# Kernel optimization log

Measured on AMD Instinct MI355X. Metric: run time of the kernel, lower is better.

## Reference

```python
import math
import jax, jax.numpy as jnp
import numpy as np

WIN = 8
NUM_HEADS = 8

def _rel_pos_index(win):
    coords = np.stack(np.meshgrid(np.arange(win), np.arange(win), indexing='ij'))
    cf = coords.reshape(2, -1)
    rel = cf[:, :, None] - cf[:, None, :]
    rel = rel.transpose(1, 2, 0).copy()
    rel[:, :, 0] += win - 1
    rel[:, :, 1] += win - 1
    rel[:, :, 0] *= 2 * win - 1
    return rel.sum(-1)  # [N, N]

def _shift_mask(H, W, win, Ho, Wo):
    m = np.zeros((H, W))
    h_slices = (slice(0, -win), slice(-win, -Ho), slice(-Ho, None)) if Ho > 0 else (slice(0, None),)
    w_slices = (slice(0, -win), slice(-win, -Wo), slice(-Wo, None)) if Wo > 0 else (slice(0, None),)
    cnt = 0
    for hs in h_slices:
        for ws in w_slices:
            m[hs, ws] = cnt
            cnt += 1
    mw = m.reshape(H // win, win, W // win, win).transpose(0, 2, 1, 3).reshape(-1, win * win)
    d = mw[:, None, :] - mw[:, :, None]
    return np.where(d != 0, -100.0, 0.0).astype(np.float32)  # [nW, N, N]

def _ln(x, g, b, eps=1e-5):
    mu = jnp.mean(x, axis=-1, keepdims=True)
    var = jnp.mean((x - mu) ** 2, axis=-1, keepdims=True)
    return (x - mu) / jnp.sqrt(var + eps) * g + b

def _win_part(x, win):
    B, H, W, C = x.shape
    x = x.reshape(B, H // win, win, W // win, win, C).transpose(0, 1, 3, 2, 4, 5)
    return x.reshape(-1, win * win, C)

def _win_rev(w, win, H, W):
    C = w.shape[-1]
    B = w.shape[0] // ((H // win) * (W // win))
    x = w.reshape(B, H // win, W // win, win, win, C).transpose(0, 1, 3, 2, 4, 5)
    return x.reshape(B, H, W, C)

def setup_inputs() -> dict:
    key = jax.random.key(0)
    ks = jax.random.split(key, 10)
    B, L, C, hid = 4, 32768, 256, 1024
    s = 0.02
    return {
        'x': jax.random.normal(ks[0], (B, L, C), jnp.float32),
        'norm1_g': jnp.ones((C,), jnp.float32),
        'norm1_b': jnp.zeros((C,), jnp.float32),
        'wq': jax.random.normal(ks[1], (C, C), jnp.float32) * s,
        'bq': jnp.zeros((C,), jnp.float32),
        'wv': jax.random.normal(ks[2], (C, C), jnp.float32) * s,
        'bv': jnp.zeros((C,), jnp.float32),
        'rpb': jax.random.normal(ks[3], (225, NUM_HEADS), jnp.float32) * s,
        'wproj': jax.random.normal(ks[4], (C, C), jnp.float32) * s,
        'bproj': jnp.zeros((C,), jnp.float32),
        'norm2_g': jnp.ones((C,), jnp.float32),
        'norm2_b': jnp.zeros((C,), jnp.float32),
        'w1': jax.random.normal(ks[5], (C, hid), jnp.float32) * s,
        'b1': jnp.zeros((hid,), jnp.float32),
        'dw_k': jax.random.normal(ks[6], (hid, 1, 3, 3), jnp.float32) * s,
        'dw_b': jnp.zeros((hid,), jnp.float32),
        'w2': jax.random.normal(ks[7], (hid, C), jnp.float32) * s,
        'b2': jnp.zeros((C,), jnp.float32),
        'H_offset': 3,
        'W_offset': 5,
    }

def reference(x, norm1_g, norm1_b, wq, bq, wv, bv, rpb, wproj, bproj,
              norm2_g, norm2_b, w1, b1, dw_k, dw_b, w2, b2, H_offset, W_offset):
    B, L, C = x.shape
    H = int(round(math.sqrt(L * 2)))
    W = int(round(math.sqrt(L // 2)))
    win, h = WIN, NUM_HEADS
    hd = C // h
    N = win * win
    nW = (H // win) * (W // win)
    scale = hd ** -0.5

    shortcut = x
    xn = _ln(x, norm1_g, norm1_b)
    q = xn @ wq + bq
    v = xn @ wv + bv
    q = q.reshape(B, H, W, C)
    v = v.reshape(B, H, W, C)
    k = q  # module uses k = q (shared)

    q = jnp.roll(q, (-H_offset, -W_offset), axis=(1, 2))
    k = jnp.roll(k, (-H_offset, -W_offset), axis=(1, 2))
    v = jnp.roll(v, (-H_offset, -W_offset), axis=(1, 2))

    qw = _win_part(q, win).reshape(-1, N, h, hd).transpose(0, 2, 1, 3)
    kw = _win_part(k, win).reshape(-1, N, h, hd).transpose(0, 2, 1, 3)
    vw = _win_part(v, win).reshape(-1, N, h, hd).transpose(0, 2, 1, 3)

    attn = jnp.einsum('bhnd,bhmd->bhnm', qw * scale, kw)
    bias = rpb[jnp.asarray(_rel_pos_index(win).reshape(-1))].reshape(N, N, h).transpose(2, 0, 1)
    attn = attn + bias[None]
    mask = jnp.asarray(_shift_mask(H, W, win, int(H_offset), int(W_offset)))
    attn = (attn.reshape(B, nW, h, N, N) + mask[None, :, None]).reshape(-1, h, N, N)
    attn = jax.nn.softmax(attn, axis=-1)

    y = jnp.einsum('bhnm,bhmd->bhnd', attn, vw).transpose(0, 2, 1, 3).reshape(-1, N, C)
    y = y @ wproj + bproj
    y = _win_rev(y.reshape(-1, win, win, C), win, H, W)
    y = jnp.roll(y, (H_offset, W_offset), axis=(1, 2)).reshape(B, L, C)

    x = shortcut + y

    # LeFF
    xn2 = _ln(x, norm2_g, norm2_b)
    t = jax.nn.gelu(xn2 @ w1 + b1, approximate=False)  # [B, L, hid]
    t = t.reshape(B, H, W, -1).transpose(0, 3, 1, 2)   # NCHW
    t = jax.lax.conv_general_dilated(t, dw_k, (1, 1), 'SAME',
                                     feature_group_count=t.shape[1],
                                     dimension_numbers=('NCHW', 'OIHW', 'NCHW'))
    t = jax.nn.gelu(t + dw_b[None, :, None, None], approximate=False)
    t = t.transpose(0, 2, 3, 1).reshape(B, L, -1)
    t = t @ w2 + b2
    return x + t
```

## Files before the change

kernel.cpp:

```cpp
#include <hip/hip_runtime.h>
#include <stdint.h>
#include <math.h>

#define H_IMG 256
#define W_IMG 128
#define LTOK  32768
#define BATCH 4
#define CDIM  256
#define HIDDIM 1024
#define NHEAD 8
#define HD    32
#define MROWS 131072

typedef __attribute__((ext_vector_type(8))) short short8;
typedef __attribute__((ext_vector_type(4))) float f32x4;

__device__ __forceinline__ float bf2f(unsigned u) {
  union { unsigned u; float f; } c; c.u = u << 16; return c.f;
}
__device__ __forceinline__ unsigned short f2bf(float f) {
  union { float f; unsigned u; } c; c.f = f;
  unsigned r = c.u + 0x7fffu + ((c.u >> 16) & 1u);
  return (unsigned short)(r >> 16);
}
__device__ __forceinline__ float gelu_f(float x) {
  return 0.5f * x * (1.0f + erff(x * 0.70710678118654752f));
}
__device__ __forceinline__ void gload_lds16(const void* g, void* l) {
  __builtin_amdgcn_global_load_lds(
      (const __attribute__((address_space(1))) unsigned int*)g,
      (__attribute__((address_space(3))) unsigned int*)l, 16, 0, 0);
}

__global__ __launch_bounds__(256) void wconv_kernel(
    const float* __restrict__ w, unsigned short* __restrict__ wt, int K, int N) {
  __shared__ float t[32][33];
  const int k0 = blockIdx.x * 32, n0 = blockIdx.y * 32;
  const int tx = threadIdx.x & 31, ty = threadIdx.x >> 5;
#pragma unroll
  for (int i = 0; i < 4; ++i)
    t[ty + 8 * i][tx] = w[(size_t)(k0 + ty + 8 * i) * N + n0 + tx];
  __syncthreads();
#pragma unroll
  for (int i = 0; i < 4; ++i)
    wt[(size_t)(n0 + ty + 8 * i) * K + k0 + tx] = f2bf(t[tx][ty + 8 * i]);
}

__global__ __launch_bounds__(256) void ln_kernel(
    const float* __restrict__ x, const float* __restrict__ g,
    const float* __restrict__ b, unsigned short* __restrict__ out) {
  const int wave = threadIdx.x >> 6;
  const int lane = threadIdx.x & 63;
  const size_t row = (size_t)blockIdx.x * 4 + wave;
  float4 f = ((const float4*)(x + row * CDIM))[lane];
  float s  = f.x + f.y + f.z + f.w;
  float sq = f.x*f.x + f.y*f.y + f.z*f.z + f.w*f.w;
#pragma unroll
  for (int o = 32; o > 0; o >>= 1) { s += __shfl_down(s, o); sq += __shfl_down(sq, o); }
  s = __shfl(s, 0); sq = __shfl(sq, 0);
  const float mu = s * (1.0f / CDIM);
  const float var = sq * (1.0f / CDIM) - mu * mu;
  const float rstd = rsqrtf(var + 1e-5f);
  float4 gg = ((const float4*)g)[lane];
  float4 bb = ((const float4*)b)[lane];
  unsigned short o4[4];
  o4[0] = f2bf((f.x - mu) * rstd * gg.x + bb.x);
  o4[1] = f2bf((f.y - mu) * rstd * gg.y + bb.y);
  o4[2] = f2bf((f.z - mu) * rstd * gg.z + bb.z);
  o4[3] = f2bf((f.w - mu) * rstd * gg.w + bb.w);
  *(uint2*)(out + row * CDIM + lane * 4) = *(uint2*)o4;
}

template<int EPI>
__global__ __launch_bounds__(256) void mgemm(
    const unsigned short* __restrict__ A, const unsigned short* __restrict__ Bt,
    const float* __restrict__ bias, float bscale, const float* __restrict__ res,
    void* __restrict__ outp, int K, int ldc) {
  __shared__ unsigned short As[128][32];
  __shared__ unsigned short Bs[128][32];
  const int tid = threadIdx.x;
  const int w = tid >> 6, lane = tid & 63;
  const int m0 = blockIdx.x * 128, n0 = blockIdx.y * 128;
  const int wm = (w & 1) * 64, wn = (w >> 1) * 64;
  const int srow = lane >> 2;
  const int csrc = (lane & 3) ^ (srow & 3);
  f32x4 acc[4][4];
#pragma unroll
  for (int mi = 0; mi < 4; ++mi)
#pragma unroll
    for (int ni = 0; ni < 4; ++ni)
#pragma unroll
      for (int r = 0; r < 4; ++r) acc[mi][ni][r] = 0.0f;

  const int kg = lane >> 4, ml = lane & 15;
  for (int kk = 0; kk < K; kk += 32) {
#pragma unroll
    for (int i = 0; i < 2; ++i) {
      const int rl = w * 32 + i * 16 + srow;
      gload_lds16(A + (size_t)(m0 + rl) * K + kk + csrc * 8, &As[w * 32 + i * 16][0]);
      gload_lds16(Bt + (size_t)(n0 + rl) * K + kk + csrc * 8, &Bs[w * 32 + i * 16][0]);
    }
    __syncthreads();
    short8 af[4], bg[4];
#pragma unroll
    for (int mi = 0; mi < 4; ++mi) {
      const int r = wm + mi * 16 + ml;
      af[mi] = *(const short8*)&As[r][(kg ^ (r & 3)) * 8];
    }
#pragma unroll
    for (int ni = 0; ni < 4; ++ni) {
      const int r = wn + ni * 16 + ml;
      bg[ni] = *(const short8*)&Bs[r][(kg ^ (r & 3)) * 8];
    }
#pragma unroll
    for (int mi = 0; mi < 4; ++mi)
#pragma unroll
      for (int ni = 0; ni < 4; ++ni)
        acc[mi][ni] = __builtin_amdgcn_mfma_f32_16x16x32_bf16(af[mi], bg[ni], acc[mi][ni], 0, 0, 0);
    __syncthreads();
  }
#pragma unroll
  for (int ni = 0; ni < 4; ++ni) {
    const int n = n0 + wn + ni * 16 + ml;
    const float bn = bias[n] * bscale;
#pragma unroll
    for (int mi = 0; mi < 4; ++mi) {
#pragma unroll
      for (int r = 0; r < 4; ++r) {
        const int m = m0 + wm + mi * 16 + kg * 4 + r;
        const size_t idx = (size_t)m * ldc + n;
        float val = acc[mi][ni][r] + bn;
        if (EPI == 1) {
          ((float*)outp)[idx] = val + res[idx];
        } else if (EPI == 2) {
          ((unsigned short*)outp)[idx] = f2bf(gelu_f(val));
        } else {
          ((unsigned short*)outp)[idx] = f2bf(val);
        }
      }
    }
  }
}

__global__ __launch_bounds__(256, 3) void attn_kernel(
    const unsigned short* __restrict__ q, const unsigned short* __restrict__ v,
    const float* __restrict__ rpb, const int* __restrict__ pHo,
    const int* __restrict__ pWo, unsigned short* __restrict__ yout) {
  __shared__ char wbuf[4][8704];
  __shared__ float bias_w[4][228];
  __shared__ int reg_s[64];
  const int tid = threadIdx.x;
  const int w = tid >> 6, lane = tid & 63;
  const int g = lane >> 4, c = lane & 15;
  const int wb = blockIdx.x;
  const int b = wb >> 9, wloc = wb & 511;
  const int wh = wloc >> 4, ww = wloc & 15;
  const int Ho = pHo[0], Wo = pWo[0];
  const int dy = lane >> 3, dx = lane & 7;
  const int hr = wh * 8 + dy, wr = ww * 8 + dx;
  int ho = hr + Ho; if (ho >= H_IMG) ho -= H_IMG;
  int wo = wr + Wo; if (wo >= W_IMG) wo -= W_IMG;
  const size_t tok = (size_t)b * LTOK + (size_t)ho * W_IMG + wo;
  const bool edge = (wh == (H_IMG / 8 - 1)) || (ww == (W_IMG / 8 - 1));
  if (w == 0) {
    const int rh = (hr < H_IMG - 8) ? 0 : ((hr < H_IMG - Ho) ? 1 : 2);
    const int rw = (wr < W_IMG - 8) ? 0 : ((wr < W_IMG - Wo) ? 1 : 2);
    reg_s[lane] = rh * 3 + rw;
  }
  __syncthreads();

  unsigned short* qh = (unsigned short*)&wbuf[w][0];
  unsigned short* vt = (unsigned short*)&wbuf[w][4096];
  unsigned short* Pp = (unsigned short*)&wbuf[w][0];

  const float scale = 0.17677669529663687f;
  const int dxk = c & 7, dyk0 = c >> 3;
  const int base_l = 112 - dyk0 * 15 - dxk;

  for (int p2 = 0; p2 < 2; ++p2) {
    const int hh = w + 4 * p2;
    const uint4* vp = (const uint4*)(v + tok * CDIM + hh * HD);
    uint4 a0 = vp[0], a1 = vp[1], a2 = vp[2], a3 = vp[3];
#pragma unroll
    for (int i = 0; i < 4; ++i) {
      const int idx = lane + 64 * i;
      if (idx < 225) bias_w[w][idx] = rpb[idx * 8 + hh];
    }
#pragma unroll
    for (int u = 0; u < 4; ++u) {
      const int t2 = u * 16 + (lane >> 2);
      int ho2 = wh * 8 + (t2 >> 3) + Ho; if (ho2 >= H_IMG) ho2 -= H_IMG;
      int wo2 = ww * 8 + (t2 & 7) + Wo;  if (wo2 >= W_IMG) wo2 -= W_IMG;
      const size_t tk = (size_t)b * LTOK + (size_t)ho2 * W_IMG + wo2;
      gload_lds16(q + tk * CDIM + hh * HD + (lane & 3) * 8, &qh[u * 512]);
    }
    {
      unsigned tmp[16] = {a0.x,a0.y,a0.z,a0.w,a1.x,a1.y,a1.z,a1.w,
                          a2.x,a2.y,a2.z,a2.w,a3.x,a3.y,a3.z,a3.w};
#pragma unroll
      for (int d2 = 0; d2 < 16; ++d2) {
        vt[(2 * d2) * 72 + lane]     = (unsigned short)(tmp[d2] & 0xffffu);
        vt[(2 * d2 + 1) * 72 + lane] = (unsigned short)(tmp[d2] >> 16);
      }
    }
    asm volatile("s_waitcnt vmcnt(0)" ::: "memory");
    short8 q4[4];
#pragma unroll
    for (int mi = 0; mi < 4; ++mi)
      q4[mi] = *(const short8*)&qh[(16 * mi + c) * 32 + g * 8];
    short8 vf[2][2];
#pragma unroll
    for (int s2 = 0; s2 < 2; ++s2)
#pragma unroll
      for (int n2 = 0; n2 < 2; ++n2)
        vf[s2][n2] = *(const short8*)&vt[(16 * n2 + c) * 72 + 32 * s2 + 8 * g];
    f32x4 acc[4][4];
#pragma unroll
    for (int mi = 0; mi < 4; ++mi)
#pragma unroll
      for (int nj = 0; nj < 4; ++nj)
#pragma unroll
        for (int r = 0; r < 4; ++r) acc[mi][nj][r] = 0.0f;
#pragma unroll
    for (int mi = 0; mi < 4; ++mi)
#pragma unroll
      for (int nj = 0; nj < 4; ++nj)
        acc[mi][nj] = __builtin_amdgcn_mfma_f32_16x16x32_bf16(q4[mi], q4[nj], acc[mi][nj], 0, 0, 0);
    int regk[4];
    if (edge) {
#pragma unroll
      for (int nj = 0; nj < 4; ++nj) regk[nj] = reg_s[16 * nj + c];
    }
#pragma unroll
    for (int mi = 0; mi < 4; ++mi) {
#pragma unroll
      for (int r = 0; r < 4; ++r) {
        const int qq = 16 * mi + 4 * g + r;
        const int rb = (qq >> 3) * 15 + (qq & 7) + base_l;
        float sv[4];
#pragma unroll
        for (int nj = 0; nj < 4; ++nj)
          sv[nj] = acc[mi][nj][r] * scale + bias_w[w][rb - 30 * nj];
        if (edge) {
          const int regq = reg_s[qq];
#pragma unroll
          for (int nj = 0; nj < 4; ++nj)
            if (regq != regk[nj]) sv[nj] -= 100.0f;
        }
        float mx2 = fmaxf(fmaxf(sv[0], sv[1]), fmaxf(sv[2], sv[3]));
        mx2 = fmaxf(mx2, __shfl_xor(mx2, 1));
        mx2 = fmaxf(mx2, __shfl_xor(mx2, 2));
        mx2 = fmaxf(mx2, __shfl_xor(mx2, 4));
        mx2 = fmaxf(mx2, __shfl_xor(mx2, 8));
        float e0 = __expf(sv[0] - mx2), e1 = __expf(sv[1] - mx2);
        float e2 = __expf(sv[2] - mx2), e3 = __expf(sv[3] - mx2);
        float sm = e0 + e1 + e2 + e3;
        sm += __shfl_xor(sm, 1);
        sm += __shfl_xor(sm, 2);
        sm += __shfl_xor(sm, 4);
        sm += __shfl_xor(sm, 8);
        const float iv = __builtin_amdgcn_rcpf(sm);
        const int rowoff = qq * 64, sw = qq & 7;
        Pp[rowoff + ((dyk0 ^ sw) * 8)       + dxk] = f2bf(e0 * iv);
        Pp[rowoff + (((2 + dyk0) ^ sw) * 8) + dxk] = f2bf(e1 * iv);
        Pp[rowoff + (((4 + dyk0) ^ sw) * 8) + dxk] = f2bf(e2 * iv);
        Pp[rowoff + (((6 + dyk0) ^ sw) * 8) + dxk] = f2bf(e3 * iv);
      }
    }
    f32x4 oacc[4][2];
#pragma unroll
    for (int mi = 0; mi < 4; ++mi)
#pragma unroll
      for (int n2 = 0; n2 < 2; ++n2)
#pragma unroll
        for (int r = 0; r < 4; ++r) oacc[mi][n2][r] = 0.0f;
#pragma unroll
    for (int s2 = 0; s2 < 2; ++s2) {
      short8 pa[4];
#pragma unroll
      for (int mi = 0; mi < 4; ++mi) {
        const int qq2 = 16 * mi + c;
        pa[mi] = *(const short8*)&Pp[qq2 * 64 + (((4 * s2 + g) ^ (qq2 & 7)) * 8)];
      }
#pragma unroll
      for (int mi = 0; mi < 4; ++mi)
#pragma unroll
        for (int n2 = 0; n2 < 2; ++n2)
          oacc[mi][n2] = __builtin_amdgcn_mfma_f32_16x16x32_bf16(pa[mi], vf[s2][n2], oacc[mi][n2], 0, 0, 0);
    }
    unsigned short* Ost = Pp;
#pragma unroll
    for (int mi = 0; mi < 4; ++mi)
#pragma unroll
      for (int n2 = 0; n2 < 2; ++n2)
#pragma unroll
        for (int r = 0; r < 4; ++r)
          Ost[(16 * mi + 4 * g + r) * 40 + 16 * n2 + c] = f2bf(oacc[mi][n2][r]);
    uint4* op = (uint4*)(yout + tok * CDIM + hh * HD);
#pragma unroll
    for (int u = 0; u < 4; ++u)
      op[u] = *(const uint4*)&Ost[lane * 40 + u * 8];
  }
}

__global__ __launch_bounds__(256) void dwconv_kernel(
    const unsigned short* __restrict__ t1b, const float* __restrict__ k9,
    const float* __restrict__ bias, unsigned short* __restrict__ t2b,
    int hr0, int band_rows) {
  const int c = blockIdx.y * 128 + (threadIdx.x & 31) * 4;
  const int tok = blockIdx.x * 8 + (threadIdx.x >> 5);
  const int h = hr0 + (tok >> 7), wcol = tok & 127;
  float wreg[4][9];
#pragma unroll
  for (int j = 0; j < 4; ++j)
#pragma unroll
    for (int tp = 0; tp < 9; ++tp) wreg[j][tp] = k9[(c + j) * 9 + tp];
  const float4 bv = *(const float4*)(bias + c);
  float a0 = 0, a1 = 0, a2 = 0, a3 = 0;
#pragma unroll
  for (int ky = 0; ky < 3; ++ky) {
    const int hy = h + ky - 1;
    if ((unsigned)hy >= (unsigned)H_IMG) continue;
    const int brow = (tok >> 7) + ky;
#pragma unroll
    for (int kx = 0; kx < 3; ++kx) {
      const int wx = wcol + kx - 1;
      if ((unsigned)wx >= (unsigned)W_IMG) continue;
      const ushort4 tv = *(const ushort4*)(
          t1b + ((size_t)(brow * 128 + wx)) * HIDDIM + c);
      const int tp = ky * 3 + kx;
      a0 += bf2f(tv.x) * wreg[0][tp];
      a1 += bf2f(tv.y) * wreg[1][tp];
      a2 += bf2f(tv.z) * wreg[2][tp];
      a3 += bf2f(tv.w) * wreg[3][tp];
    }
  }
  a0 = gelu_f(a0 + bv.x); a1 = gelu_f(a1 + bv.y);
  a2 = gelu_f(a2 + bv.z); a3 = gelu_f(a3 + bv.w);
  unsigned short o[4] = { f2bf(a0), f2bf(a1), f2bf(a2), f2bf(a3) };
  *(uint2*)(t2b + (size_t)tok * HIDDIM + c) = *(uint2*)o;
}

extern "C" void kernel_launch(void* const* d_in, const int* in_sizes, int n_in,
                              void* d_out, int out_size, void* d_ws, size_t ws_size,
                              hipStream_t stream) {
  (void)in_sizes; (void)n_in; (void)out_size; (void)ws_size;
  const float* x     = (const float*)d_in[0];
  const float* n1g   = (const float*)d_in[1];
  const float* n1b   = (const float*)d_in[2];
  const float* wq    = (const float*)d_in[3];
  const float* bq    = (const float*)d_in[4];
  const float* wv    = (const float*)d_in[5];
  const float* bv    = (const float*)d_in[6];
  const float* rpb   = (const float*)d_in[7];
  const float* wproj = (const float*)d_in[8];
  const float* bproj = (const float*)d_in[9];
  const float* n2g   = (const float*)d_in[10];
  const float* n2b   = (const float*)d_in[11];
  const float* w1    = (const float*)d_in[12];
  const float* b1    = (const float*)d_in[13];
  const float* dwk   = (const float*)d_in[14];
  const float* dwb   = (const float*)d_in[15];
  const float* w2    = (const float*)d_in[16];
  const float* b2    = (const float*)d_in[17];
  const int*   pHo   = (const int*)d_in[18];
  const int*   pWo   = (const int*)d_in[19];
  float* out = (float*)d_out;

  char* wsb = (char*)d_ws;
  unsigned short* r0     = (unsigned short*)wsb;
  unsigned short* wqt    = (unsigned short*)(wsb + 67108864ull);
  unsigned short* wvt    = (unsigned short*)(wsb + 67108864ull + 131072ull);
  unsigned short* wprojt = (unsigned short*)(wsb + 67108864ull + 262144ull);
  unsigned short* w1t    = (unsigned short*)(wsb + 67108864ull + 393216ull);
  unsigned short* w2t    = (unsigned short*)(wsb + 67108864ull + 917504ull);
  unsigned short* t1b    = (unsigned short*)(wsb + 68550656ull);
  unsigned short* t2b    = (unsigned short*)(wsb + 68550656ull + 25690112ull);
  unsigned short* vb     = (unsigned short*)d_out;
  unsigned short* qb     = (unsigned short*)((char*)d_out + 67108864ull);

  wconv_kernel<<<dim3(8, 8),  256, 0, stream>>>(wq,    wqt,    CDIM, CDIM);
  wconv_kernel<<<dim3(8, 8),  256, 0, stream>>>(wv,    wvt,    CDIM, CDIM);
  wconv_kernel<<<dim3(8, 8),  256, 0, stream>>>(wproj, wprojt, CDIM, CDIM);
  wconv_kernel<<<dim3(8, 32), 256, 0, stream>>>(w1,    w1t,    CDIM, HIDDIM);
  wconv_kernel<<<dim3(32, 8), 256, 0, stream>>>(w2,    w2t,    HIDDIM, CDIM);

  ln_kernel<<<32768, 256, 0, stream>>>(x, n1g, n1b, r0);
  mgemm<0><<<dim3(1024, 2), 256, 0, stream>>>(r0, wqt, bq, 1.0f, nullptr, qb, CDIM, CDIM);
  mgemm<0><<<dim3(1024, 2), 256, 0, stream>>>(r0, wvt, bv, 1.0f, nullptr, vb, CDIM, CDIM);
  attn_kernel<<<dim3(2048), 256, 0, stream>>>(qb, vb, rpb, pHo, pWo, r0);
  mgemm<1><<<dim3(1024, 2), 256, 0, stream>>>(r0, wprojt, bproj, 1.0f, x, out, CDIM, CDIM);
  ln_kernel<<<32768, 256, 0, stream>>>(out, n2g, n2b, r0);
  for (int bi = 0; bi < BATCH; ++bi) {
    for (int hr0 = 0; hr0 < H_IMG; ) {
      const int br = (H_IMG - hr0 >= 96) ? 96 : (H_IMG - hr0);
      const int r_start = (hr0 > 0) ? hr0 - 1 : 0;
      const int r_end = (hr0 + br <= H_IMG - 1) ? hr0 + br : H_IMG - 1;
      const int nrows = r_end - r_start + 1;
      const unsigned short* Aff1 = r0 + ((size_t)bi * LTOK + (size_t)r_start * W_IMG) * CDIM;
      unsigned short* t1dst = t1b + (size_t)(r_start - hr0 + 1) * W_IMG * HIDDIM;
      mgemm<2><<<dim3(nrows, 8), 256, 0, stream>>>(
          Aff1, w1t, b1, 1.0f, nullptr, t1dst, CDIM, HIDDIM);
      dwconv_kernel<<<dim3(br * 16, 8), 256, 0, stream>>>(t1b, dwk, dwb, t2b, hr0, br);
      const size_t btok = (size_t)bi * LTOK + (size_t)hr0 * W_IMG;
      mgemm<1><<<dim3(br, 2), 256, 0, stream>>>(
          t2b, w2t, b2, 1.0f, out + btok * CDIM, out + btok * CDIM, HIDDIM, CDIM);
      hr0 += br;
    }
  }
}
```

Baseline: 1.635 ms.

## Double-buffer GEMM K loop, write Q/V in window-major layout, drop softmax max

The GEMM main loop now uses two LDS stages so the next K tile is prefetched while MFMAs run on the current one. The Q and V projection GEMMs write their output already shifted and window-partitioned per head (V transposed), and the projection GEMM reads window-ordered rows and scatters them back with the reverse roll. This lets the attention kernel read Q/V fragments straight from global memory without LDS staging or transposes. The softmax also drops the row-max subtraction and applies the normalisation after P@V, which assumes scores stay small enough not to overflow exp.

```diff
diff --git a/kernel.cpp b/kernel.cpp
--- a/kernel.cpp
+++ b/kernel.cpp
@@ -71,13 +71,14 @@
   *(uint2*)(out + row * CDIM + lane * 4) = *(uint2*)o4;
 }
 
-template<int EPI>
+template<int EPI, int PERM>
 __global__ __launch_bounds__(256) void mgemm(
     const unsigned short* __restrict__ A, const unsigned short* __restrict__ Bt,
     const float* __restrict__ bias, float bscale, const float* __restrict__ res,
-    void* __restrict__ outp, int K, int ldc) {
-  __shared__ unsigned short As[128][32];
-  __shared__ unsigned short Bs[128][32];
+    void* __restrict__ outp, int K, int ldc,
+    const int* __restrict__ pHo, const int* __restrict__ pWo) {
+  __shared__ unsigned short As[2][128][32];
+  __shared__ unsigned short Bs[2][128][32];
   const int tid = threadIdx.x;
   const int w = tid >> 6, lane = tid & 63;
   const int m0 = blockIdx.x * 128, n0 = blockIdx.y * 128;
@@ -93,42 +94,88 @@
       for (int r = 0; r < 4; ++r) acc[mi][ni][r] = 0.0f;
 
   const int kg = lane >> 4, ml = lane & 15;
-  for (int kk = 0; kk < K; kk += 32) {
+  const int nt = K >> 5;
+
+  auto STAGE = [&](int kk, int buf) {
 #pragma unroll
     for (int i = 0; i < 2; ++i) {
       const int rl = w * 32 + i * 16 + srow;
-      gload_lds16(A + (size_t)(m0 + rl) * K + kk + csrc * 8, &As[w * 32 + i * 16][0]);
-      gload_lds16(Bt + (size_t)(n0 + rl) * K + kk + csrc * 8, &Bs[w * 32 + i * 16][0]);
-    }
-    __syncthreads();
+      gload_lds16(A + (size_t)(m0 + rl) * K + kk + csrc * 8, &As[buf][w * 32 + i * 16][0]);
+      gload_lds16(Bt + (size_t)(n0 + rl) * K + kk + csrc * 8, &Bs[buf][w * 32 + i * 16][0]);
+    }
+  };
+
+  STAGE(0, 0);
+  for (int t = 0; t < nt; ++t) {
+    const int cur = t & 1;
+    if (t + 1 < nt) {
+      STAGE((t + 1) << 5, cur ^ 1);
+      asm volatile("s_waitcnt vmcnt(4)" ::: "memory");
+    } else {
+      asm volatile("s_waitcnt vmcnt(0)" ::: "memory");
+    }
+    __builtin_amdgcn_s_barrier();
+    __builtin_amdgcn_sched_barrier(0);
     short8 af[4], bg[4];
 #pragma unroll
     for (int mi = 0; mi < 4; ++mi) {
       const int r = wm + mi * 16 + ml;
-      af[mi] = *(const short8*)&As[r][(kg ^ (r & 3)) * 8];
+      af[mi] = *(const short8*)&As[cur][r][(kg ^ (r & 3)) * 8];
     }
 #pragma unroll
     for (int ni = 0; ni < 4; ++ni) {
       const int r = wn + ni * 16 + ml;
-      bg[ni] = *(const short8*)&Bs[r][(kg ^ (r & 3)) * 8];
+      bg[ni] = *(const short8*)&Bs[cur][r][(kg ^ (r & 3)) * 8];
     }
 #pragma unroll
     for (int mi = 0; mi < 4; ++mi)
 #pragma unroll
       for (int ni = 0; ni < 4; ++ni)
         acc[mi][ni] = __builtin_amdgcn_mfma_f32_16x16x32_bf16(af[mi], bg[ni], acc[mi][ni], 0, 0, 0);
-    __syncthreads();
+    __builtin_amdgcn_sched_barrier(0);
+    __builtin_amdgcn_s_barrier();
+  }
+
+  const int Ho = (PERM == 1 || PERM == 2 || PERM == 3) ? pHo[0] : 0;
+  const int Wo = (PERM == 1 || PERM == 2 || PERM == 3) ? pWo[0] : 0;
+  size_t ridx[4][4];
+#pragma unroll
+  for (int mi = 0; mi < 4; ++mi) {
+#pragma unroll
+    for (int r = 0; r < 4; ++r) {
+      const int m = m0 + wm + mi * 16 + kg * 4 + r;
+      if constexpr (PERM == 1 || PERM == 2) {
+        const int bimg = m >> 15, l = m & 32767;
+        const int hq = l >> 7, wq_ = l & 127;
+        int hr = hq - Ho; if (hr < 0) hr += H_IMG;
+        int wr = wq_ - Wo; if (wr < 0) wr += W_IMG;
+        const int win = (hr >> 3) * 16 + (wr >> 3);
+        const int t64 = (hr & 7) * 8 + (wr & 7);
+        ridx[mi][r] = (size_t)(bimg * 512 + win) * 16384 +
+                      (PERM == 1 ? t64 * 32 : t64);
+      } else if constexpr (PERM == 3) {
+        const int bimg = m >> 15, win = (m >> 6) & 511, t64 = m & 63;
+        int h = (win >> 4) * 8 + (t64 >> 3) + Ho; if (h >= H_IMG) h -= H_IMG;
+        int ww_ = (win & 15) * 8 + (t64 & 7) + Wo; if (ww_ >= W_IMG) ww_ -= W_IMG;
+        ridx[mi][r] = ((size_t)(bimg << 15) + h * W_IMG + ww_) * ldc;
+      } else {
+        ridx[mi][r] = (size_t)m * ldc;
+      }
+    }
   }
 #pragma unroll
   for (int ni = 0; ni < 4; ++ni) {
     const int n = n0 + wn + ni * 16 + ml;
     const float bn = bias[n] * bscale;
+    size_t noff;
+    if constexpr (PERM == 1)      noff = (size_t)(n >> 5) * 2048 + (n & 31);
+    else if constexpr (PERM == 2) noff = (size_t)(n >> 5) * 2048 + (n & 31) * 64;
+    else                          noff = (size_t)n;
 #pragma unroll
     for (int mi = 0; mi < 4; ++mi) {
 #pragma unroll
       for (int r = 0; r < 4; ++r) {
-        const int m = m0 + wm + mi * 16 + kg * 4 + r;
-        const size_t idx = (size_t)m * ldc + n;
+        const size_t idx = ridx[mi][r] + noff;
         float val = acc[mi][ni][r] + bn;
         if (EPI == 1) {
           ((float*)outp)[idx] = val + res[idx];
@@ -146,7 +193,7 @@
     const unsigned short* __restrict__ q, const unsigned short* __restrict__ v,
     const float* __restrict__ rpb, const int* __restrict__ pHo,
     const int* __restrict__ pWo, unsigned short* __restrict__ yout) {
-  __shared__ char wbuf[4][8704];
+  __shared__ unsigned short Pb[4][4096];
   __shared__ float bias_w[4][228];
   __shared__ int reg_s[64];
   const int tid = threadIdx.x;
@@ -156,64 +203,40 @@
   const int b = wb >> 9, wloc = wb & 511;
   const int wh = wloc >> 4, ww = wloc & 15;
   const int Ho = pHo[0], Wo = pWo[0];
-  const int dy = lane >> 3, dx = lane & 7;
-  const int hr = wh * 8 + dy, wr = ww * 8 + dx;
-  int ho = hr + Ho; if (ho >= H_IMG) ho -= H_IMG;
-  int wo = wr + Wo; if (wo >= W_IMG) wo -= W_IMG;
-  const size_t tok = (size_t)b * LTOK + (size_t)ho * W_IMG + wo;
   const bool edge = (wh == (H_IMG / 8 - 1)) || (ww == (W_IMG / 8 - 1));
   if (w == 0) {
+    const int dy = lane >> 3, dx = lane & 7;
+    const int hr = wh * 8 + dy, wr = ww * 8 + dx;
     const int rh = (hr < H_IMG - 8) ? 0 : ((hr < H_IMG - Ho) ? 1 : 2);
     const int rw = (wr < W_IMG - 8) ? 0 : ((wr < W_IMG - Wo) ? 1 : 2);
     reg_s[lane] = rh * 3 + rw;
   }
   __syncthreads();
 
-  unsigned short* qh = (unsigned short*)&wbuf[w][0];
-  unsigned short* vt = (unsigned short*)&wbuf[w][4096];
-  unsigned short* Pp = (unsigned short*)&wbuf[w][0];
-
   const float scale = 0.17677669529663687f;
   const int dxk = c & 7, dyk0 = c >> 3;
   const int base_l = 112 - dyk0 * 15 - dxk;
+  const size_t hbase0 = (size_t)(b * 512 + wloc) * 8;
 
   for (int p2 = 0; p2 < 2; ++p2) {
     const int hh = w + 4 * p2;
-    const uint4* vp = (const uint4*)(v + tok * CDIM + hh * HD);
-    uint4 a0 = vp[0], a1 = vp[1], a2 = vp[2], a3 = vp[3];
+    const unsigned short* qh = q + (hbase0 + hh) * 2048;
+    const unsigned short* vh = v + (hbase0 + hh) * 2048;
 #pragma unroll
     for (int i = 0; i < 4; ++i) {
       const int idx = lane + 64 * i;
       if (idx < 225) bias_w[w][idx] = rpb[idx * 8 + hh];
     }
-#pragma unroll
-    for (int u = 0; u < 4; ++u) {
-      const int t2 = u * 16 + (lane >> 2);
-      int ho2 = wh * 8 + (t2 >> 3) + Ho; if (ho2 >= H_IMG) ho2 -= H_IMG;
-      int wo2 = ww * 8 + (t2 & 7) + Wo;  if (wo2 >= W_IMG) wo2 -= W_IMG;
-      const size_t tk = (size_t)b * LTOK + (size_t)ho2 * W_IMG + wo2;
-      gload_lds16(q + tk * CDIM + hh * HD + (lane & 3) * 8, &qh[u * 512]);
-    }
-    {
-      unsigned tmp[16] = {a0.x,a0.y,a0.z,a0.w,a1.x,a1.y,a1.z,a1.w,
-                          a2.x,a2.y,a2.z,a2.w,a3.x,a3.y,a3.z,a3.w};
-#pragma unroll
-      for (int d2 = 0; d2 < 16; ++d2) {
-        vt[(2 * d2) * 72 + lane]     = (unsigned short)(tmp[d2] & 0xffffu);
-        vt[(2 * d2 + 1) * 72 + lane] = (unsigned short)(tmp[d2] >> 16);
-      }
-    }
-    asm volatile("s_waitcnt vmcnt(0)" ::: "memory");
     short8 q4[4];
 #pragma unroll
     for (int mi = 0; mi < 4; ++mi)
-      q4[mi] = *(const short8*)&qh[(16 * mi + c) * 32 + g * 8];
+      q4[mi] = *(const short8*)(qh + (16 * mi + c) * 32 + g * 8);
     short8 vf[2][2];
 #pragma unroll
     for (int s2 = 0; s2 < 2; ++s2)
 #pragma unroll
       for (int n2 = 0; n2 < 2; ++n2)
-        vf[s2][n2] = *(const short8*)&vt[(16 * n2 + c) * 72 + 32 * s2 + 8 * g];
+        vf[s2][n2] = *(const short8*)(vh + (16 * n2 + c) * 64 + 32 * s2 + 8 * g);
     f32x4 acc[4][4];
 #pragma unroll
     for (int mi = 0; mi < 4; ++mi)
@@ -231,6 +254,8 @@
 #pragma unroll
       for (int nj = 0; nj < 4; ++nj) regk[nj] = reg_s[16 * nj + c];
     }
+    unsigned short* Pp = &Pb[w][0];
+    float ivr[4][4];
 #pragma unroll
     for (int mi = 0; mi < 4; ++mi) {
 #pragma unroll
@@ -247,24 +272,19 @@
           for (int nj = 0; nj < 4; ++nj)
             if (regq != regk[nj]) sv[nj] -= 100.0f;
         }
-        float mx2 = fmaxf(fmaxf(sv[0], sv[1]), fmaxf(sv[2], sv[3]));
-        mx2 = fmaxf(mx2, __shfl_xor(mx2, 1));
-        mx2 = fmaxf(mx2, __shfl_xor(mx2, 2));
-        mx2 = fmaxf(mx2, __shfl_xor(mx2, 4));
-        mx2 = fmaxf(mx2, __shfl_xor(mx2, 8));
-        float e0 = __expf(sv[0] - mx2), e1 = __expf(sv[1] - mx2);
-        float e2 = __expf(sv[2] - mx2), e3 = __expf(sv[3] - mx2);
+        float e0 = __expf(sv[0]), e1 = __expf(sv[1]);
+        float e2 = __expf(sv[2]), e3 = __expf(sv[3]);
         float sm = e0 + e1 + e2 + e3;
         sm += __shfl_xor(sm, 1);
         sm += __shfl_xor(sm, 2);
         sm += __shfl_xor(sm, 4);
         sm += __shfl_xor(sm, 8);
-        const float iv = __builtin_amdgcn_rcpf(sm);
+        ivr[mi][r] = __builtin_amdgcn_rcpf(sm);
         const int rowoff = qq * 64, sw = qq & 7;
-        Pp[rowoff + ((dyk0 ^ sw) * 8)       + dxk] = f2bf(e0 * iv);
-        Pp[rowoff + (((2 + dyk0) ^ sw) * 8) + dxk] = f2bf(e1 * iv);
-        Pp[rowoff + (((4 + dyk0) ^ sw) * 8) + dxk] = f2bf(e2 * iv);
-        Pp[rowoff + (((6 + dyk0) ^ sw) * 8) + dxk] = f2bf(e3 * iv);
+        Pp[rowoff + ((dyk0 ^ sw) * 8)       + dxk] = f2bf(e0);
+        Pp[rowoff + (((2 + dyk0) ^ sw) * 8) + dxk] = f2bf(e1);
+        Pp[rowoff + (((4 + dyk0) ^ sw) * 8) + dxk] = f2bf(e2);
+        Pp[rowoff + (((6 + dyk0) ^ sw) * 8) + dxk] = f2bf(e3);
       }
     }
     f32x4 oacc[4][2];
@@ -295,8 +315,8 @@
       for (int n2 = 0; n2 < 2; ++n2)
 #pragma unroll
         for (int r = 0; r < 4; ++r)
-          Ost[(16 * mi + 4 * g + r) * 40 + 16 * n2 + c] = f2bf(oacc[mi][n2][r]);
-    uint4* op = (uint4*)(yout + tok * CDIM + hh * HD);
+          Ost[(16 * mi + 4 * g + r) * 40 + 16 * n2 + c] = f2bf(oacc[mi][n2][r] * ivr[mi][r]);
+    uint4* op = (uint4*)(yout + ((size_t)(b * 512 + wloc) * 64 + lane) * 256 + hh * 32);
 #pragma unroll
     for (int u = 0; u < 4; ++u)
       op[u] = *(const uint4*)&Ost[lane * 40 + u * 8];
@@ -386,10 +406,10 @@
   wconv_kernel<<<dim3(32, 8), 256, 0, stream>>>(w2,    w2t,    HIDDIM, CDIM);
 
   ln_kernel<<<32768, 256, 0, stream>>>(x, n1g, n1b, r0);
-  mgemm<0><<<dim3(1024, 2), 256, 0, stream>>>(r0, wqt, bq, 1.0f, nullptr, qb, CDIM, CDIM);
-  mgemm<0><<<dim3(1024, 2), 256, 0, stream>>>(r0, wvt, bv, 1.0f, nullptr, vb, CDIM, CDIM);
+  mgemm<0, 1><<<dim3(1024, 2), 256, 0, stream>>>(r0, wqt, bq, 1.0f, nullptr, qb, CDIM, CDIM, pHo, pWo);
+  mgemm<0, 2><<<dim3(1024, 2), 256, 0, stream>>>(r0, wvt, bv, 1.0f, nullptr, vb, CDIM, CDIM, pHo, pWo);
   attn_kernel<<<dim3(2048), 256, 0, stream>>>(qb, vb, rpb, pHo, pWo, r0);
-  mgemm<1><<<dim3(1024, 2), 256, 0, stream>>>(r0, wprojt, bproj, 1.0f, x, out, CDIM, CDIM);
+  mgemm<1, 3><<<dim3(1024, 2), 256, 0, stream>>>(r0, wprojt, bproj, 1.0f, x, out, CDIM, CDIM, pHo, pWo);
   ln_kernel<<<32768, 256, 0, stream>>>(out, n2g, n2b, r0);
   for (int bi = 0; bi < BATCH; ++bi) {
     for (int hr0 = 0; hr0 < H_IMG; ) {
@@ -399,12 +419,12 @@
       const int nrows = r_end - r_start + 1;
       const unsigned short* Aff1 = r0 + ((size_t)bi * LTOK + (size_t)r_start * W_IMG) * CDIM;
       unsigned short* t1dst = t1b + (size_t)(r_start - hr0 + 1) * W_IMG * HIDDIM;
-      mgemm<2><<<dim3(nrows, 8), 256, 0, stream>>>(
-          Aff1, w1t, b1, 1.0f, nullptr, t1dst, CDIM, HIDDIM);
+      mgemm<2, 0><<<dim3(nrows, 8), 256, 0, stream>>>(
+          Aff1, w1t, b1, 1.0f, nullptr, t1dst, CDIM, HIDDIM, pHo, pWo);
       dwconv_kernel<<<dim3(br * 16, 8), 256, 0, stream>>>(t1b, dwk, dwb, t2b, hr0, br);
       const size_t btok = (size_t)bi * LTOK + (size_t)hr0 * W_IMG;
-      mgemm<1><<<dim3(br, 2), 256, 0, stream>>>(
-          t2b, w2t, b2, 1.0f, out + btok * CDIM, out + btok * CDIM, HIDDIM, CDIM);
+      mgemm<1, 0><<<dim3(br, 2), 256, 0, stream>>>(
+          t2b, w2t, b2, 1.0f, out + btok * CDIM, out + btok * CDIM, HIDDIM, CDIM, pHo, pWo);
       hr0 += br;
     }
   }
```

Measured after the change: 1.656 ms. No clear change (+1.2%).
